# Performance work log

Measured on AMD Instinct MI355X. Metric: run time of the kernel, lower is better.

## Reference

```python
import jax, jax.numpy as jnp
import numpy as np
from jax import lax

K_SIZE = 9
PAD = K_SIZE // 2


def _diag_pool(x):
    """Fixed diagonal box-filter conv with kernel[o,c,i,j] = (i==j)/k.
    Since every (out,in) channel pair uses the same diagonal kernel, the
    dense conv collapses to: channel-sum -> diagonal k-tap average,
    broadcast to all output channels. Matches F.conv2d(x, kernel,
    padding='same') exactly for the main-diagonal kernel (types=False).
    """
    B, C, H, W = x.shape
    s = x.sum(axis=1)  # [B, H, W] channel sum
    sp = jnp.pad(s, ((0, 0), (PAD, PAD), (PAD, PAD)))
    acc = jnp.zeros_like(s)
    for d in range(K_SIZE):  # fixed small loop over the k diagonal taps
        acc = acc + lax.dynamic_slice(sp, (0, d, d), (B, H, W))
    d = acc / K_SIZE  # [B, H, W]
    return jnp.broadcast_to(d[:, None], (B, C, H, W))


def setup_inputs() -> dict:
    key = jax.random.key(0)
    kx, kw = jax.random.split(key)
    x = jax.random.normal(kx, (4, 32, 720, 720), dtype=jnp.float32)
    conv_w = jax.random.normal(kw, (32, 32, 3, 1), dtype=jnp.float32) * 0.05
    return {"x": x, "conv_w": conv_w}


def reference(x, conv_w):
    diapool = lax.stop_gradient(_diag_pool(x))  # torch.no_grad() block
    # 3x1 conv, padding (1,0), no bias
    out = lax.conv_general_dilated(
        diapool, conv_w,
        window_strides=(1, 1),
        padding=((1, 1), (0, 0)),
        dimension_numbers=("NCHW", "OIHW", "NCHW"),
    )
    return out
```

## Files before the change

### kernel.cpp

```cpp
#include <hip/hip_runtime.h>

#define Bn 4
#define Cn 32
#define Hn 720
#define Wn 720
#define W4 (Wn / 4)
#define HW (Hn * Wn)
#define NPIX (Bn * Hn * Wn)
#define NV (NPIX / 4)

__global__ void wsum_kernel(const float* __restrict__ conv_w,
                            float* __restrict__ wsum) {
    int t = threadIdx.x;
    if (t < 96) {
        int o = t / 3, kh = t - o * 3;
        float acc = 0.f;
        #pragma unroll
        for (int i = 0; i < Cn; ++i)
            acc += conv_w[(o * Cn + i) * 3 + kh];
        wsum[t] = acc;
    }
}

__global__ void csum_kernel(const float* __restrict__ x,
                            float* __restrict__ s) {
    int idx = blockIdx.x * blockDim.x + threadIdx.x;
    if (idx >= NV) return;
    int b = idx / (Hn * W4);
    int rem = idx - b * (Hn * W4);
    const float4* xp = (const float4*)x + (size_t)b * Cn * Hn * W4 + rem;
    float4 acc = make_float4(0.f, 0.f, 0.f, 0.f);
    #pragma unroll 8
    for (int c = 0; c < Cn; ++c) {
        float4 v = xp[(size_t)c * Hn * W4];
        acc.x += v.x; acc.y += v.y; acc.z += v.z; acc.w += v.w;
    }
    ((float4*)s)[idx] = acc;
}

__global__ void diag_kernel(const float* __restrict__ s,
                            float* __restrict__ d) {
    int idx = blockIdx.x * blockDim.x + threadIdx.x;
    if (idx >= NV) return;
    int b = idx / (Hn * W4);
    int rem = idx - b * (Hn * W4);
    int h = rem / W4;
    int w0 = (rem - h * W4) * 4;
    const float* sb = s + (size_t)b * HW;
    float acc0 = 0.f, acc1 = 0.f, acc2 = 0.f, acc3 = 0.f;
    #pragma unroll
    for (int t = -4; t <= 4; ++t) {
        int hh = h + t;
        if (hh < 0 || hh >= Hn) continue;
        const float* row = sb + (size_t)hh * Wn;
        int ww = w0 + t;
        if (ww >= 0 && ww < Wn)         acc0 += row[ww];
        if (ww + 1 >= 0 && ww + 1 < Wn) acc1 += row[ww + 1];
        if (ww + 2 >= 0 && ww + 2 < Wn) acc2 += row[ww + 2];
        if (ww + 3 >= 0 && ww + 3 < Wn) acc3 += row[ww + 3];
    }
    const float inv9 = 1.f / 9.f;
    ((float4*)d)[idx] = make_float4(acc0 * inv9, acc1 * inv9,
                                    acc2 * inv9, acc3 * inv9);
}

__global__ void conv_kernel(const float* __restrict__ d,
                            const float* __restrict__ wsum,
                            float* __restrict__ out) {
    __shared__ float ws[96];
    if (threadIdx.x < 96) ws[threadIdx.x] = wsum[threadIdx.x];
    __syncthreads();
    int idx = blockIdx.x * blockDim.x + threadIdx.x;
    if (idx >= NV) return;
    int b = idx / (Hn * W4);
    int rem = idx - b * (Hn * W4);
    int h = rem / W4;
    int w4 = rem - h * W4;
    const float4* db = (const float4*)d + (size_t)b * Hn * W4;
    float4 z = make_float4(0.f, 0.f, 0.f, 0.f);
    float4 dm = (h > 0)      ? db[(size_t)(h - 1) * W4 + w4] : z;
    float4 dc =                db[(size_t)h * W4 + w4];
    float4 dp = (h < Hn - 1) ? db[(size_t)(h + 1) * W4 + w4] : z;
    float4* ob = (float4*)out + (size_t)b * Cn * Hn * W4 + (size_t)h * W4 + w4;
    #pragma unroll
    for (int o = 0; o < Cn; ++o) {
        float k0 = ws[o * 3 + 0], k1 = ws[o * 3 + 1], k2 = ws[o * 3 + 2];
        float4 r;
        r.x = k0 * dm.x + k1 * dc.x + k2 * dp.x;
        r.y = k0 * dm.y + k1 * dc.y + k2 * dp.y;
        r.z = k0 * dm.z + k1 * dc.z + k2 * dp.z;
        r.w = k0 * dm.w + k1 * dc.w + k2 * dp.w;
        ob[(size_t)o * Hn * W4] = r;
    }
}

extern "C" void kernel_launch(void* const* d_in, const int* in_sizes, int n_in,
                              void* d_out, int out_size, void* d_ws, size_t ws_size,
                              hipStream_t stream) {
    const float* x = (const float*)d_in[0];
    const float* conv_w = (const float*)d_in[1];
    float* out = (float*)d_out;

    float* s    = (float*)d_ws;
    float* dbuf = s + NPIX;
    float* wsum = dbuf + NPIX;

    wsum_kernel<<<1, 96, 0, stream>>>(conv_w, wsum);

    const int threads = 256;
    const int blocks = (NV + threads - 1) / threads;
    csum_kernel<<<blocks, threads, 0, stream>>>(x, s);
    diag_kernel<<<blocks, threads, 0, stream>>>(s, dbuf);
    conv_kernel<<<blocks, threads, 0, stream>>>(dbuf, wsum, out);
}
```

Before: 471.5 us.

## Fuse diagonal pooling into conv kernel using zero-padded channel-sum buffer

Writes the channel sum into a zero-padded buffer so the 9-tap diagonal average can be computed without bounds checks. The pooling is then fused into the 3x1 conv kernel, removing one kernel launch and one intermediate round trip. It also switches to nontemporal loads and stores on the large input and output streams. In exchange it adds a memset of the padded buffer each call and recomputes three pooled rows per thread.

```diff
diff --git a/kernel.cpp b/kernel.cpp
--- a/kernel.cpp
+++ b/kernel.cpp
@@ -5,9 +5,13 @@
 #define Hn 720
 #define Wn 720
 #define W4 (Wn / 4)
-#define HW (Hn * Wn)
-#define NPIX (Bn * Hn * Wn)
-#define NV (NPIX / 4)
+#define NV (Bn * Hn * W4)
+
+#define PH (Hn + 10)
+#define PW (Wn + 8)
+#define SPAD_ELEMS (Bn * PH * PW)
+
+typedef float v4 __attribute__((ext_vector_type(4)));
 
 __global__ void wsum_kernel(const float* __restrict__ conv_w,
                             float* __restrict__ wsum) {
@@ -23,50 +27,27 @@
 }
 
 __global__ void csum_kernel(const float* __restrict__ x,
-                            float* __restrict__ s) {
-    int idx = blockIdx.x * blockDim.x + threadIdx.x;
-    if (idx >= NV) return;
-    int b = idx / (Hn * W4);
-    int rem = idx - b * (Hn * W4);
-    const float4* xp = (const float4*)x + (size_t)b * Cn * Hn * W4 + rem;
-    float4 acc = make_float4(0.f, 0.f, 0.f, 0.f);
-    #pragma unroll 8
-    for (int c = 0; c < Cn; ++c) {
-        float4 v = xp[(size_t)c * Hn * W4];
-        acc.x += v.x; acc.y += v.y; acc.z += v.z; acc.w += v.w;
-    }
-    ((float4*)s)[idx] = acc;
-}
-
-__global__ void diag_kernel(const float* __restrict__ s,
-                            float* __restrict__ d) {
+                            float* __restrict__ sp) {
     int idx = blockIdx.x * blockDim.x + threadIdx.x;
     if (idx >= NV) return;
     int b = idx / (Hn * W4);
     int rem = idx - b * (Hn * W4);
     int h = rem / W4;
-    int w0 = (rem - h * W4) * 4;
-    const float* sb = s + (size_t)b * HW;
-    float acc0 = 0.f, acc1 = 0.f, acc2 = 0.f, acc3 = 0.f;
-    #pragma unroll
-    for (int t = -4; t <= 4; ++t) {
-        int hh = h + t;
-        if (hh < 0 || hh >= Hn) continue;
-        const float* row = sb + (size_t)hh * Wn;
-        int ww = w0 + t;
-        if (ww >= 0 && ww < Wn)         acc0 += row[ww];
-        if (ww + 1 >= 0 && ww + 1 < Wn) acc1 += row[ww + 1];
-        if (ww + 2 >= 0 && ww + 2 < Wn) acc2 += row[ww + 2];
-        if (ww + 3 >= 0 && ww + 3 < Wn) acc3 += row[ww + 3];
+    int w4 = rem - h * W4;
+    const v4* xp = (const v4*)x + (size_t)b * Cn * Hn * W4 + rem;
+    v4 acc = {0.f, 0.f, 0.f, 0.f};
+    #pragma unroll 8
+    for (int c = 0; c < Cn; ++c) {
+        v4 v = __builtin_nontemporal_load(&xp[(size_t)c * Hn * W4]);
+        acc += v;
     }
-    const float inv9 = 1.f / 9.f;
-    ((float4*)d)[idx] = make_float4(acc0 * inv9, acc1 * inv9,
-                                    acc2 * inv9, acc3 * inv9);
+    v4* dst = (v4*)(sp + ((size_t)b * PH + 5 + h) * PW + 4) + w4;
+    *dst = acc;
 }
 
-__global__ void conv_kernel(const float* __restrict__ d,
-                            const float* __restrict__ wsum,
-                            float* __restrict__ out) {
+__global__ void fused_kernel(const float* __restrict__ sp,
+                             const float* __restrict__ wsum,
+                             float* __restrict__ out) {
     __shared__ float ws[96];
     if (threadIdx.x < 96) ws[threadIdx.x] = wsum[threadIdx.x];
     __syncthreads();
@@ -76,21 +57,41 @@
     int rem = idx - b * (Hn * W4);
     int h = rem / W4;
     int w4 = rem - h * W4;
-    const float4* db = (const float4*)d + (size_t)b * Hn * W4;
-    float4 z = make_float4(0.f, 0.f, 0.f, 0.f);
-    float4 dm = (h > 0)      ? db[(size_t)(h - 1) * W4 + w4] : z;
-    float4 dc =                db[(size_t)h * W4 + w4];
-    float4 dp = (h < Hn - 1) ? db[(size_t)(h + 1) * W4 + w4] : z;
-    float4* ob = (float4*)out + (size_t)b * Cn * Hn * W4 + (size_t)h * W4 + w4;
+    const float* srow = sp + ((size_t)b * PH + 5 + h) * PW + 4 + 4 * w4;
+
+    float a0[4] = {0,0,0,0}, a1[4] = {0,0,0,0}, a2[4] = {0,0,0,0};
+    #pragma unroll
+    for (int r = -5; r <= 5; ++r) {
+        const float* p = srow + (long)r * PW - 4;
+        v4 u0 = *(const v4*)p;
+        v4 u1 = *(const v4*)(p + 4);
+        v4 u2 = *(const v4*)(p + 8);
+        float v[12] = {u0[0],u0[1],u0[2],u0[3],
+                       u1[0],u1[1],u1[2],u1[3],
+                       u2[0],u2[1],u2[2],u2[3]};
+        #pragma unroll
+        for (int j = 0; j < 3; ++j) {
+            const int t = r + 1 - j;
+            if (t >= -4 && t <= 4) {
+                float* a = (j == 0) ? a0 : (j == 1) ? a1 : a2;
+                #pragma unroll
+                for (int l = 0; l < 4; ++l) a[l] += v[4 + l + t];
+            }
+        }
+    }
+    if (h == 0) { a0[0]=a0[1]=a0[2]=a0[3]=0.f; }
+    if (h == Hn - 1) { a2[0]=a2[1]=a2[2]=a2[3]=0.f; }
+
+    const float inv9 = 1.f / 9.f;
+    float* ob = out + (size_t)b * Cn * Hn * Wn + (size_t)h * Wn + 4 * w4;
     #pragma unroll
     for (int o = 0; o < Cn; ++o) {
-        float k0 = ws[o * 3 + 0], k1 = ws[o * 3 + 1], k2 = ws[o * 3 + 2];
-        float4 r;
-        r.x = k0 * dm.x + k1 * dc.x + k2 * dp.x;
-        r.y = k0 * dm.y + k1 * dc.y + k2 * dp.y;
-        r.z = k0 * dm.z + k1 * dc.z + k2 * dp.z;
-        r.w = k0 * dm.w + k1 * dc.w + k2 * dp.w;
-        ob[(size_t)o * Hn * W4] = r;
+        float k0 = ws[3*o] * inv9, k1 = ws[3*o+1] * inv9, k2 = ws[3*o+2] * inv9;
+        v4 r;
+        #pragma unroll
+        for (int l = 0; l < 4; ++l)
+            r[l] = k0 * a0[l] + k1 * a1[l] + k2 * a2[l];
+        __builtin_nontemporal_store(r, (v4*)(ob + (size_t)o * Hn * Wn));
     }
 }
 
@@ -101,15 +102,15 @@
     const float* conv_w = (const float*)d_in[1];
     float* out = (float*)d_out;
 
-    float* s    = (float*)d_ws;
-    float* dbuf = s + NPIX;
-    float* wsum = dbuf + NPIX;
+    float* sp   = (float*)d_ws;
+    float* wsum = sp + SPAD_ELEMS;
+
+    hipMemsetAsync(sp, 0, (size_t)SPAD_ELEMS * sizeof(float), stream);
 
     wsum_kernel<<<1, 96, 0, stream>>>(conv_w, wsum);
 
     const int threads = 256;
     const int blocks = (NV + threads - 1) / threads;
-    csum_kernel<<<blocks, threads, 0, stream>>>(x, s);
-    diag_kernel<<<blocks, threads, 0, stream>>>(s, dbuf);
-    conv_kernel<<<blocks, threads, 0, stream>>>(dbuf, wsum, out);
+    csum_kernel<<<blocks, threads, 0, stream>>>(x, sp);
+    fused_kernel<<<blocks, threads, 0, stream>>>(sp, wsum, out);
 }
```

Measured after the change: 423.4 us. 1.11x faster.
